# Kernel optimization log

Measured on AMD Instinct MI355X. Metric: run time of the kernel, lower is better.

Reference implementation:

```python
import jax, jax.numpy as jnp
import numpy as np

B, S, T, N, D, L = 8192, 10, 3, 65536, 128, 2  # batch, neigh len, node types, table size, embed_d, layers
NEG_SLOPE = 0.01  # torch LeakyReLU default


def setup_inputs() -> dict:
    key = jax.random.key(0)
    ks = jax.random.split(key, 6)
    return {
        "emb": jax.random.normal(ks[0], (T, N, D), jnp.float32) * 0.02,
        "Wih": jax.random.normal(ks[1], (L, T, D, D), jnp.float32) / np.sqrt(D).astype(np.float32),
        "Whh": jax.random.normal(ks[2], (L, T, D, D), jnp.float32) / np.sqrt(D).astype(np.float32),
        "bih": jnp.full((L, T, D), 0.1, jnp.float32),
        "bhh": jnp.full((L, T, D), 0.1, jnp.float32),
        "w_att": jax.random.normal(ks[3], (L, 2 * D), jnp.float32) / np.sqrt(2 * D).astype(np.float32),
        "ids": jax.random.randint(ks[4], (B,), 0, N),
        "neigh_idx": jax.random.randint(ks[5], (T, B, S), 0, N),
    }


def _rnn_mean(x, Wih_l, Whh_l, bih_l, bhh_l):
    """x: [T,B,S,D] neighbor embeds. torch nn.RNN(tanh): h_s = tanh(x_s@Wih^T + bih + h@Whh^T + bhh).
    Returns mean of all hidden states over time: [T,B,D]."""
    xs = jnp.moveaxis(x, 2, 0)  # [S, T, B, D]
    h0 = jnp.zeros((T, B, D), x.dtype)

    def step(h, x_s):
        h = jnp.tanh(jnp.einsum('tbd,ted->tbe', x_s, Wih_l) + bih_l[:, None, :]
                     + jnp.einsum('tbd,ted->tbe', h, Whh_l) + bhh_l[:, None, :])
        return h, h

    _, hs = jax.lax.scan(step, h0, xs)  # [S, T, B, D]
    return hs.mean(axis=0)


def reference(emb, Wih, Whh, bih, bhh, w_att, ids, neigh_idx):
    cur = emb[0][ids]  # [B, D] target node type = 0
    # per-type neighbor gather from base embedding tables (same each layer, as in source)
    neigh = jax.vmap(lambda e, i: e[i])(emb, neigh_idx)  # [T, B, S, D]
    for l in range(L):
        agg = _rnn_mean(neigh, Wih[l], Whh[l], bih[l], bhh[l])  # [T, B, D]
        cands = jnp.moveaxis(jnp.concatenate([cur[None], agg], axis=0), 0, 1)  # [B, 1+T, D]
        feat = jnp.concatenate(
            [jnp.broadcast_to(cur[:, None, :], cands.shape), cands], axis=-1)  # [B, 1+T, 2D]
        scores = feat @ w_att[l]  # [B, 1+T]
        w = jax.nn.softmax(scores, axis=1)[..., None]
        cur = jax.nn.leaky_relu(jnp.sum(w * cands, axis=1), NEG_SLOPE)
    return cur
```

## Files before the change

kernel.cpp:

```cpp
#include <hip/hip_runtime.h>
#include <hip/hip_bf16.h>

#define NB   8192
#define NS   10
#define NT   3
#define NN   65536
#define ND   128
#define NL   2
#define ROWS 32

typedef __attribute__((ext_vector_type(8))) short bf16x8;
typedef __attribute__((ext_vector_type(4))) float f32x4;

__device__ __forceinline__ unsigned int pk2(float lo, float hi) {
    unsigned int r;
    asm("v_cvt_pk_bf16_f32 %0, %1, %2" : "=v"(r) : "v"(lo), "v"(hi));
    return r;
}
__device__ __forceinline__ float tanh_f(float x) {
    float e, r;
    asm("v_exp_f32 %0, %1" : "=v"(e) : "v"(x * 2.88539004f));
    asm("v_rcp_f32 %0, %1" : "=v"(r) : "v"(e + 1.0f));
    return fmaf(-2.0f, r, 1.0f);
}
__device__ __forceinline__ void bar_lgkm() {
    asm volatile("s_waitcnt lgkmcnt(0)\n\ts_barrier" ::: "memory");
}

__global__ __launch_bounds__(512)
void rnn_kernel(const float* __restrict__ emb, const float* __restrict__ Wih,
                const float* __restrict__ Whh, const float* __restrict__ bih,
                const float* __restrict__ bhh, const int* __restrict__ nidx,
                float* __restrict__ agg)
{
    __shared__ __align__(16) char lds[6 * 8192];

    const int bid = blockIdx.x;
    const int t   = bid / (NB / ROWS);
    const int b0  = (bid % (NB / ROWS)) * ROWS;

    const int tid  = threadIdx.x;
    const int wv   = tid >> 6;
    const int lay  = wv >> 2;
    const int lane = tid & 63;
    const int l16  = lane & 15;
    const int lg   = lane >> 4;
    const int e0   = (wv & 3) * 32;
    const int rx   = l16 & 7;

    char* xb = lds;
    char* hb = lds + 16384 + lay * 16384;

    const int srow  = tid >> 4;
    const int sq    = tid & 15;
    const int xaddr = srow * 256 + ((sq ^ (srow & 7)) << 4);

    const int* ip = nidx + ((size_t)t * NB + b0 + srow) * NS;
    int idx_nxt = ip[1];

    float4 P0, P1;
    {
        const float* src = emb + ((size_t)t * NN + ip[0]) * ND + sq * 8;
        P0 = *(const float4*)(src);
        P1 = *(const float4*)(src + 4);
    }

    const float* Wih_lt = Wih + (size_t)(lay * NT + t) * ND * ND;
    const float* Whh_lt = Whh + (size_t)(lay * NT + t) * ND * ND;
    const float* bih_lt = bih + (size_t)(lay * NT + t) * ND;
    const float* bhh_lt = bhh + (size_t)(lay * NT + t) * ND;

    bf16x8 Af[2][8];
    #pragma unroll
    for (int mt = 0; mt < 2; ++mt) {
        #pragma unroll
        for (int kc = 0; kc < 8; ++kc) {
            const float* Wsrc = (kc < 4) ? Wih_lt : Whh_lt;
            const float* srcp = Wsrc + (size_t)(e0 + mt * 16 + l16) * ND + (kc & 3) * 32 + lg * 8;
            float4 p0 = *(const float4*)(srcp);
            float4 p1 = *(const float4*)(srcp + 4);
            int4 a;
            a.x = (int)pk2(p0.x, p0.y);
            a.y = (int)pk2(p0.z, p0.w);
            a.z = (int)pk2(p1.x, p1.y);
            a.w = (int)pk2(p1.z, p1.w);
            Af[mt][kc] = *(bf16x8*)&a;
        }
    }

    f32x4 biasv[2];
    #pragma unroll
    for (int mt = 0; mt < 2; ++mt) {
        int e = e0 + mt * 16 + lg * 4;
        float4 bi = *(const float4*)(bih_lt + e);
        float4 bh = *(const float4*)(bhh_lt + e);
        biasv[mt][0] = bi.x + bh.x;
        biasv[mt][1] = bi.y + bh.y;
        biasv[mt][2] = bi.z + bh.z;
        biasv[mt][3] = bi.w + bh.w;
    }

    const int rowb = l16 * 256;
    int rdch[4];
    #pragma unroll
    for (int c = 0; c < 4; ++c)
        rdch[c] = ((c * 4 + lg) ^ rx) << 4;
    const int hw0 = ((((e0 >> 3) + (lg >> 1)) ^ rx) << 4) + (lg & 1) * 8;
    const int hw1 = ((((e0 >> 3) + 2 + (lg >> 1)) ^ rx) << 4) + (lg & 1) * 8;

    f32x4 zero4; zero4[0] = 0.f; zero4[1] = 0.f; zero4[2] = 0.f; zero4[3] = 0.f;
    f32x4 Ag[2][2];
    #pragma unroll
    for (int nt = 0; nt < 2; ++nt) { Ag[nt][0] = zero4; Ag[nt][1] = zero4; }

    #pragma unroll 1
    for (int s = 0; s < NS; ++s) {
        const int par  = (s & 1) * 8192;
        const int ppar = 8192 - par;

        {
            int4 pk;
            pk.x = (int)pk2(P0.x, P0.y);
            pk.y = (int)pk2(P0.z, P0.w);
            pk.z = (int)pk2(P1.x, P1.y);
            pk.w = (int)pk2(P1.z, P1.w);
            *(int4*)(xb + xaddr + par) = pk;
        }
        if (s + 1 < NS) {
            const float* src = emb + ((size_t)t * NN + idx_nxt) * ND + sq * 8;
            P0 = *(const float4*)(src);
            P1 = *(const float4*)(src + 4);
            idx_nxt = ip[(s + 2 < NS) ? s + 2 : 0];
        }
        bar_lgkm();

        f32x4 acc[2][2];
        #pragma unroll
        for (int nt = 0; nt < 2; ++nt) { acc[nt][0] = biasv[0]; acc[nt][1] = biasv[1]; }

        #pragma unroll
        for (int nt = 0; nt < 2; ++nt)
            #pragma unroll
            for (int c = 0; c < 4; ++c) {
                bf16x8 bf = *(const bf16x8*)(xb + rowb + rdch[c] + nt * 4096 + par);
                acc[nt][0] = __builtin_amdgcn_mfma_f32_16x16x32_bf16(Af[0][c], bf, acc[nt][0], 0, 0, 0);
                acc[nt][1] = __builtin_amdgcn_mfma_f32_16x16x32_bf16(Af[1][c], bf, acc[nt][1], 0, 0, 0);
            }
        if (s > 0) {
            #pragma unroll
            for (int nt = 0; nt < 2; ++nt)
                #pragma unroll
                for (int c = 0; c < 4; ++c) {
                    bf16x8 bf = *(const bf16x8*)(hb + rowb + rdch[c] + nt * 4096 + ppar);
                    acc[nt][0] = __builtin_amdgcn_mfma_f32_16x16x32_bf16(Af[0][c + 4], bf, acc[nt][0], 0, 0, 0);
                    acc[nt][1] = __builtin_amdgcn_mfma_f32_16x16x32_bf16(Af[1][c + 4], bf, acc[nt][1], 0, 0, 0);
                }
        }

        #pragma unroll
        for (int nt = 0; nt < 2; ++nt) {
            f32x4 h0, h1;
            #pragma unroll
            for (int i = 0; i < 4; ++i) {
                h0[i] = tanh_f(acc[nt][0][i]);
                h1[i] = tanh_f(acc[nt][1][i]);
            }
            Ag[nt][0] += h0;
            Ag[nt][1] += h1;
            int2 pk0, pk1;
            pk0.x = (int)pk2(h0[0], h0[1]);
            pk0.y = (int)pk2(h0[2], h0[3]);
            pk1.x = (int)pk2(h1[0], h1[1]);
            pk1.y = (int)pk2(h1[2], h1[3]);
            *(int2*)(hb + rowb + hw0 + nt * 4096 + par) = pk0;
            *(int2*)(hb + rowb + hw1 + nt * 4096 + par) = pk1;
        }
    }

    float* aggp = agg + ((size_t)(lay * NT + t) * NB + b0) * ND;
    #pragma unroll
    for (int nt = 0; nt < 2; ++nt)
        #pragma unroll
        for (int mt = 0; mt < 2; ++mt) {
            f32x4 v = Ag[nt][mt] * 0.1f;
            *(f32x4*)(aggp + (size_t)(nt * 16 + l16) * ND + e0 + mt * 16 + lg * 4) = v;
        }
}

__global__ __launch_bounds__(256)
void att_kernel(const float* __restrict__ emb, const int* __restrict__ ids,
                const float* __restrict__ w_att, const float* __restrict__ agg,
                float* __restrict__ cur, const int l)
{
    const int wid  = threadIdx.x >> 6;
    const int lane = threadIdx.x & 63;
    const int b    = blockIdx.x * 4 + wid;

    const float* waH  = w_att + l * 2 * ND;
    const float* waT  = waH + ND;
    const float* crow = (l == 0) ? (emb + (size_t)ids[b] * ND) : (cur + (size_t)b * ND);
    const float* ab   = agg + ((size_t)(l * NT) * NB + b) * ND;

    const float c1 = crow[lane], c2 = crow[lane + 64];
    const float h1 = waH[lane],  h2 = waH[lane + 64];
    const float t1 = waT[lane],  t2 = waT[lane + 64];
    float g1[3], g2[3];
    #pragma unroll
    for (int tt = 0; tt < 3; ++tt) {
        g1[tt] = ab[(size_t)tt * NB * ND + lane];
        g2[tt] = ab[(size_t)tt * NB * ND + lane + 64];
    }

    float dH = c1 * h1 + c2 * h2;
    float dc = c1 * t1 + c2 * t2;
    float d0 = g1[0] * t1 + g2[0] * t2;
    float d1 = g1[1] * t1 + g2[1] * t2;
    float d2 = g1[2] * t1 + g2[2] * t2;
    #pragma unroll
    for (int off = 32; off > 0; off >>= 1) {
        dH += __shfl_xor(dH, off);
        dc += __shfl_xor(dc, off);
        d0 += __shfl_xor(d0, off);
        d1 += __shfl_xor(d1, off);
        d2 += __shfl_xor(d2, off);
    }

    float s0 = dH + dc, s1 = dH + d0, s2 = dH + d1, s3 = dH + d2;
    float m  = fmaxf(fmaxf(s0, s1), fmaxf(s2, s3));
    float q0 = __expf(s0 - m), q1 = __expf(s1 - m), q2 = __expf(s2 - m), q3 = __expf(s3 - m);
    float inv = __fdividef(1.0f, q0 + q1 + q2 + q3);
    float w0 = q0 * inv, w1 = q1 * inv, w2 = q2 * inv, w3 = q3 * inv;

    float o1 = w0 * c1 + w1 * g1[0] + w2 * g1[1] + w3 * g1[2];
    float o2 = w0 * c2 + w1 * g2[0] + w2 * g2[1] + w3 * g2[2];
    o1 = (o1 > 0.f) ? o1 : 0.01f * o1;
    o2 = (o2 > 0.f) ? o2 : 0.01f * o2;

    float* orow = cur + (size_t)b * ND;
    orow[lane]      = o1;
    orow[lane + 64] = o2;
}

extern "C" void kernel_launch(void* const* d_in, const int* in_sizes, int n_in,
                              void* d_out, int out_size, void* d_ws, size_t ws_size,
                              hipStream_t stream)
{
    const float* emb  = (const float*)d_in[0];
    const float* Wih  = (const float*)d_in[1];
    const float* Whh  = (const float*)d_in[2];
    const float* bih  = (const float*)d_in[3];
    const float* bhh  = (const float*)d_in[4];
    const float* watt = (const float*)d_in[5];
    const int*   ids  = (const int*)d_in[6];
    const int*   nidx = (const int*)d_in[7];

    float* cur = (float*)d_out;
    float* agg = (float*)d_ws;

    rnn_kernel<<<dim3(NT * (NB / ROWS)), dim3(512), 0, stream>>>(emb, Wih, Whh, bih, bhh, nidx, agg);
    att_kernel<<<dim3(NB / 4), dim3(256), 0, stream>>>(emb, ids, watt, agg, cur, 0);
    att_kernel<<<dim3(NB / 4), dim3(256), 0, stream>>>(emb, ids, watt, agg, cur, 1);
}
```

Baseline: 78.45 us.

## Prefetch neighbor embeddings two steps ahead and unroll RNN loop by two

The RNN time loop is unrolled by two with fixed LDS buffer parities, and the embedding gather is deepened to two outstanding rows (A/B register sets) so global loads have a full extra step to land. MFMA sections are wrapped in s_setprio to favor matrix issue over other waves. The cost is more live registers (two extra float4 pairs), which could affect occupancy.

```diff
diff --git a/kernel.cpp b/kernel.cpp
--- a/kernel.cpp
+++ b/kernel.cpp
@@ -56,14 +56,19 @@
     const int xaddr = srow * 256 + ((sq ^ (srow & 7)) << 4);
 
     const int* ip = nidx + ((size_t)t * NB + b0 + srow) * NS;
-    int idx_nxt = ip[1];
-
-    float4 P0, P1;
+    const float* ebase = emb + (size_t)t * NN * ND + sq * 8;
+
+    float4 PA0, PA1, PB0, PB1;
     {
-        const float* src = emb + ((size_t)t * NN + ip[0]) * ND + sq * 8;
-        P0 = *(const float4*)(src);
-        P1 = *(const float4*)(src + 4);
-    }
+        const float* sa = ebase + (size_t)ip[0] * ND;
+        PA0 = *(const float4*)(sa);
+        PA1 = *(const float4*)(sa + 4);
+        const float* sb = ebase + (size_t)ip[1] * ND;
+        PB0 = *(const float4*)(sb);
+        PB1 = *(const float4*)(sb + 4);
+    }
+    int idx_a = ip[2];
+    int idx_b = ip[3];
 
     const float* Wih_lt = Wih + (size_t)(lay * NT + t) * ND * ND;
     const float* Whh_lt = Whh + (size_t)(lay * NT + t) * ND * ND;
@@ -114,66 +119,127 @@
     for (int nt = 0; nt < 2; ++nt) { Ag[nt][0] = zero4; Ag[nt][1] = zero4; }
 
     #pragma unroll 1
-    for (int s = 0; s < NS; ++s) {
-        const int par  = (s & 1) * 8192;
-        const int ppar = 8192 - par;
-
+    for (int s2 = 0; s2 < NS / 2; ++s2) {
         {
             int4 pk;
-            pk.x = (int)pk2(P0.x, P0.y);
-            pk.y = (int)pk2(P0.z, P0.w);
-            pk.z = (int)pk2(P1.x, P1.y);
-            pk.w = (int)pk2(P1.z, P1.w);
-            *(int4*)(xb + xaddr + par) = pk;
-        }
-        if (s + 1 < NS) {
-            const float* src = emb + ((size_t)t * NN + idx_nxt) * ND + sq * 8;
-            P0 = *(const float4*)(src);
-            P1 = *(const float4*)(src + 4);
-            idx_nxt = ip[(s + 2 < NS) ? s + 2 : 0];
+            pk.x = (int)pk2(PA0.x, PA0.y);
+            pk.y = (int)pk2(PA0.z, PA0.w);
+            pk.z = (int)pk2(PA1.x, PA1.y);
+            pk.w = (int)pk2(PA1.z, PA1.w);
+            *(int4*)(xb + xaddr) = pk;
+        }
+        if (s2 < NS / 2 - 1) {
+            const float* src = ebase + (size_t)idx_a * ND;
+            PA0 = *(const float4*)(src);
+            PA1 = *(const float4*)(src + 4);
+            idx_a = ip[(2 * s2 + 4 < NS) ? 2 * s2 + 4 : 0];
         }
         bar_lgkm();
 
-        f32x4 acc[2][2];
-        #pragma unroll
-        for (int nt = 0; nt < 2; ++nt) { acc[nt][0] = biasv[0]; acc[nt][1] = biasv[1]; }
-
-        #pragma unroll
-        for (int nt = 0; nt < 2; ++nt)
-            #pragma unroll
-            for (int c = 0; c < 4; ++c) {
-                bf16x8 bf = *(const bf16x8*)(xb + rowb + rdch[c] + nt * 4096 + par);
-                acc[nt][0] = __builtin_amdgcn_mfma_f32_16x16x32_bf16(Af[0][c], bf, acc[nt][0], 0, 0, 0);
-                acc[nt][1] = __builtin_amdgcn_mfma_f32_16x16x32_bf16(Af[1][c], bf, acc[nt][1], 0, 0, 0);
+        {
+            f32x4 acc[2][2];
+            #pragma unroll
+            for (int nt = 0; nt < 2; ++nt) { acc[nt][0] = biasv[0]; acc[nt][1] = biasv[1]; }
+
+            __builtin_amdgcn_s_setprio(1);
+            #pragma unroll
+            for (int nt = 0; nt < 2; ++nt)
+                #pragma unroll
+                for (int c = 0; c < 4; ++c) {
+                    bf16x8 bf = *(const bf16x8*)(xb + rowb + rdch[c] + nt * 4096);
+                    acc[nt][0] = __builtin_amdgcn_mfma_f32_16x16x32_bf16(Af[0][c], bf, acc[nt][0], 0, 0, 0);
+                    acc[nt][1] = __builtin_amdgcn_mfma_f32_16x16x32_bf16(Af[1][c], bf, acc[nt][1], 0, 0, 0);
+                }
+            if (s2 > 0) {
+                #pragma unroll
+                for (int nt = 0; nt < 2; ++nt)
+                    #pragma unroll
+                    for (int c = 0; c < 4; ++c) {
+                        bf16x8 bf = *(const bf16x8*)(hb + rowb + rdch[c] + nt * 4096 + 8192);
+                        acc[nt][0] = __builtin_amdgcn_mfma_f32_16x16x32_bf16(Af[0][c + 4], bf, acc[nt][0], 0, 0, 0);
+                        acc[nt][1] = __builtin_amdgcn_mfma_f32_16x16x32_bf16(Af[1][c + 4], bf, acc[nt][1], 0, 0, 0);
+                    }
             }
-        if (s > 0) {
+            __builtin_amdgcn_s_setprio(0);
+
+            #pragma unroll
+            for (int nt = 0; nt < 2; ++nt) {
+                f32x4 h0, h1;
+                #pragma unroll
+                for (int i = 0; i < 4; ++i) {
+                    h0[i] = tanh_f(acc[nt][0][i]);
+                    h1[i] = tanh_f(acc[nt][1][i]);
+                }
+                Ag[nt][0] += h0;
+                Ag[nt][1] += h1;
+                int2 pk0, pk1;
+                pk0.x = (int)pk2(h0[0], h0[1]);
+                pk0.y = (int)pk2(h0[2], h0[3]);
+                pk1.x = (int)pk2(h1[0], h1[1]);
+                pk1.y = (int)pk2(h1[2], h1[3]);
+                *(int2*)(hb + rowb + hw0 + nt * 4096) = pk0;
+                *(int2*)(hb + rowb + hw1 + nt * 4096) = pk1;
+            }
+        }
+
+        {
+            int4 pk;
+            pk.x = (int)pk2(PB0.x, PB0.y);
+            pk.y = (int)pk2(PB0.z, PB0.w);
+            pk.z = (int)pk2(PB1.x, PB1.y);
+            pk.w = (int)pk2(PB1.z, PB1.w);
+            *(int4*)(xb + xaddr + 8192) = pk;
+        }
+        if (s2 < NS / 2 - 1) {
+            const float* src = ebase + (size_t)idx_b * ND;
+            PB0 = *(const float4*)(src);
+            PB1 = *(const float4*)(src + 4);
+            idx_b = ip[(2 * s2 + 5 < NS) ? 2 * s2 + 5 : 0];
+        }
+        bar_lgkm();
+
+        {
+            f32x4 acc[2][2];
+            #pragma unroll
+            for (int nt = 0; nt < 2; ++nt) { acc[nt][0] = biasv[0]; acc[nt][1] = biasv[1]; }
+
+            __builtin_amdgcn_s_setprio(1);
             #pragma unroll
             for (int nt = 0; nt < 2; ++nt)
                 #pragma unroll
                 for (int c = 0; c < 4; ++c) {
-                    bf16x8 bf = *(const bf16x8*)(hb + rowb + rdch[c] + nt * 4096 + ppar);
+                    bf16x8 bf = *(const bf16x8*)(xb + rowb + rdch[c] + nt * 4096 + 8192);
+                    acc[nt][0] = __builtin_amdgcn_mfma_f32_16x16x32_bf16(Af[0][c], bf, acc[nt][0], 0, 0, 0);
+                    acc[nt][1] = __builtin_amdgcn_mfma_f32_16x16x32_bf16(Af[1][c], bf, acc[nt][1], 0, 0, 0);
+                }
+            #pragma unroll
+            for (int nt = 0; nt < 2; ++nt)
+                #pragma unroll
+                for (int c = 0; c < 4; ++c) {
+                    bf16x8 bf = *(const bf16x8*)(hb + rowb + rdch[c] + nt * 4096);
                     acc[nt][0] = __builtin_amdgcn_mfma_f32_16x16x32_bf16(Af[0][c + 4], bf, acc[nt][0], 0, 0, 0);
                     acc[nt][1] = __builtin_amdgcn_mfma_f32_16x16x32_bf16(Af[1][c + 4], bf, acc[nt][1], 0, 0, 0);
                 }
-        }
-
-        #pragma unroll
-        for (int nt = 0; nt < 2; ++nt) {
-            f32x4 h0, h1;
-            #pragma unroll
-            for (int i = 0; i < 4; ++i) {
-                h0[i] = tanh_f(acc[nt][0][i]);
-                h1[i] = tanh_f(acc[nt][1][i]);
+            __builtin_amdgcn_s_setprio(0);
+
+            #pragma unroll
+            for (int nt = 0; nt < 2; ++nt) {
+                f32x4 h0, h1;
+                #pragma unroll
+                for (int i = 0; i < 4; ++i) {
+                    h0[i] = tanh_f(acc[nt][0][i]);
+                    h1[i] = tanh_f(acc[nt][1][i]);
+                }
+                Ag[nt][0] += h0;
+                Ag[nt][1] += h1;
+                int2 pk0, pk1;
+                pk0.x = (int)pk2(h0[0], h0[1]);
+                pk0.y = (int)pk2(h0[2], h0[3]);
+                pk1.x = (int)pk2(h1[0], h1[1]);
+                pk1.y = (int)pk2(h1[2], h1[3]);
+                *(int2*)(hb + rowb + hw0 + nt * 4096 + 8192) = pk0;
+                *(int2*)(hb + rowb + hw1 + nt * 4096 + 8192) = pk1;
             }
-            Ag[nt][0] += h0;
-            Ag[nt][1] += h1;
-            int2 pk0, pk1;
-            pk0.x = (int)pk2(h0[0], h0[1]);
-            pk0.y = (int)pk2(h0[2], h0[3]);
-            pk1.x = (int)pk2(h1[0], h1[1]);
-            pk1.y = (int)pk2(h1[2], h1[3]);
-            *(int2*)(hb + rowb + hw0 + nt * 4096 + par) = pk0;
-            *(int2*)(hb + rowb + hw1 + nt * 4096 + par) = pk1;
         }
     }
 
```

Result: no change. 77.28 us (-1.5%).
